# Kernel tuning notes

Hardware: AMD Instinct MI355X
Metric: run time of the kernel (lower is better)

## Reference

```python
import jax, jax.numpy as jnp
import numpy as np

B, N, HID, H, DH, NB = 4, 4096, 768, 12, 64, 266
EPS = 1e-4


def softmax_kernel(data, proj, is_query):
    # data: [B,H,N,DH], proj: [NB,DH]. FAVOR+ positive softmax features.
    d = data.shape[-1]
    ratio = proj.shape[0] ** -0.5
    dn = d ** -0.25  # data normalizer
    data_dash = jnp.einsum('bhnd,jd->bhnj', data * dn, proj)  # [B,H,N,NB]
    diag = 0.5 * jnp.sum((data * dn) ** 2, axis=-1, keepdims=True)  # [B,H,N,1]
    if is_query:
        m = jnp.max(data_dash, axis=-1, keepdims=True)
    else:
        m = jnp.max(data_dash, axis=(-1, -2), keepdims=True)
    return ratio * (jnp.exp(data_dash - diag - m) + EPS)


def setup_inputs() -> dict:
    key = jax.random.key(0)
    ks = jax.random.split(key, 8)
    s = HID ** -0.5
    return {
        'hidden_states': jax.random.normal(ks[0], (B, N, HID), jnp.float32),
        'Wq': jax.random.normal(ks[1], (HID, HID), jnp.float32) * s,
        'bq': jnp.zeros((HID,), jnp.float32),
        'Wk': jax.random.normal(ks[2], (HID, HID), jnp.float32) * s,
        'bk': jnp.zeros((HID,), jnp.float32),
        'Wv': jax.random.normal(ks[3], (HID, HID), jnp.float32) * s,
        'bv': jnp.zeros((HID,), jnp.float32),
        'proj': jax.random.normal(ks[4], (NB, DH), jnp.float32),
    }


def reference(hidden_states, Wq, bq, Wk, bk, Wv, bv, proj):
    def heads(x):  # [B,N,HID] -> [B,H,N,DH]
        return x.reshape(B, N, H, DH).transpose(0, 2, 1, 3)

    q = heads(hidden_states @ Wq.T + bq)
    k = heads(hidden_states @ Wk.T + bk)
    v = heads(hidden_states @ Wv.T + bv)

    qp = softmax_kernel(q, proj, True)   # [B,H,N,NB]
    kp = softmax_kernel(k, proj, False)  # [B,H,N,NB]

    # non-causal linear attention: out = q' (k'^T v) / (q' sum_n k')
    k_sum = jnp.sum(kp, axis=2)                               # [B,H,NB]
    d_inv = 1.0 / jnp.einsum('bhnj,bhj->bhn', qp, k_sum)      # [B,H,N]
    ctx = jnp.einsum('bhnj,bhnd->bhjd', kp, v)                # [B,H,NB,DH]
    out = jnp.einsum('bhnj,bhjd->bhnd', qp, ctx) * d_inv[..., None]

    return out.transpose(0, 2, 1, 3).reshape(B, N, HID)
```

## Files before the change

kernel.cpp:

```cpp
#include <hip/hip_runtime.h>
#include <hip/hip_bf16.h>
#include <stdint.h>

#define B_   4
#define N_   4096
#define HID_ 768
#define H_   12
#define DH_  64
#define NB_  266
#define NBP_ 288
#define EPS_ 1e-4f

typedef unsigned short u16;
typedef __attribute__((ext_vector_type(8))) short short8;
typedef __attribute__((ext_vector_type(4))) float floatx4;

__device__ __forceinline__ u16 f2b(float f) {
  __hip_bfloat16 h = __float2bfloat16(f);
  return *reinterpret_cast<u16*>(&h);
}
__device__ __forceinline__ float b2f(u16 u) {
  union { unsigned u; float f; } x; x.u = ((unsigned)u) << 16; return x.f;
}
__device__ __forceinline__ unsigned fmap(float x) {
  unsigned u = __float_as_uint(x);
  return (u & 0x80000000u) ? ~u : (u | 0x80000000u);
}
__device__ __forceinline__ float funmap(unsigned u) {
  unsigned b = (u & 0x80000000u) ? (u & 0x7FFFFFFFu) : ~u;
  return __uint_as_float(b);
}

__global__ void k_convert(const float* __restrict__ src, u16* __restrict__ dst, int n) {
  int i = blockIdx.x * blockDim.x + threadIdx.x;
  int stride = gridDim.x * blockDim.x;
  for (; i < n; i += stride) dst[i] = f2b(src[i]);
}

__global__ void k_prep_proj(const float* __restrict__ proj, u16* __restrict__ dst) {
  int i = blockIdx.x * 256 + threadIdx.x;
  if (i >= NBP_ * DH_) return;
  int j = i / DH_, d = i - j * DH_;
  float v = (j < NB_) ? proj[j * DH_ + d] * 0.35355339059327373f : 0.f;
  dst[i] = f2b(v);
}

__global__ void k_init(float* __restrict__ zf, unsigned* __restrict__ mbuf, int nf) {
  int i = blockIdx.x * 256 + threadIdx.x;
  if (i < nf) zf[i] = 0.f;
  if (i < B_ * H_) mbuf[i] = 0u;
}

__global__ __launch_bounds__(256) void k_qkv(
    const u16* __restrict__ hsb, const u16* __restrict__ wb,
    const float* __restrict__ bq, const float* __restrict__ bk, const float* __restrict__ bv,
    u16* __restrict__ qb, u16* __restrict__ kb, u16* __restrict__ vb) {
  __shared__ u16 At[128][40];
  __shared__ u16 Bt[128][40];
  const int bm = blockIdx.x, bn = blockIdx.y;
  const int m0 = bm * 128;
  const int sel = bn / 6;
  const int or0 = (bn % 6) * 128;
  const u16* W = wb + (size_t)sel * HID_ * HID_;
  const int t = threadIdx.x, lane = t & 63, wv = t >> 6;
  const int wr = (wv >> 1) * 64, wc = (wv & 1) * 64;
  const int lm = lane & 15, lq = lane >> 4;
  floatx4 acc[4][4];
#pragma unroll
  for (int i = 0; i < 4; i++)
#pragma unroll
    for (int j = 0; j < 4; j++) acc[i][j] = (floatx4){0.f, 0.f, 0.f, 0.f};

  for (int k0 = 0; k0 < HID_; k0 += 32) {
    __syncthreads();
#pragma unroll
    for (int i = 0; i < 2; i++) {
      int c = t + i * 256;
      int r = c >> 2, off = (c & 3) * 8;
      *(uint4*)&At[r][off] = *(const uint4*)(hsb + (size_t)(m0 + r) * HID_ + k0 + off);
      *(uint4*)&Bt[r][off] = *(const uint4*)(W + (size_t)(or0 + r) * HID_ + k0 + off);
    }
    __syncthreads();
    short8 af[4], bfr[4];
#pragma unroll
    for (int mt = 0; mt < 4; mt++) af[mt] = *(const short8*)&At[wr + mt * 16 + lm][lq * 8];
#pragma unroll
    for (int nt = 0; nt < 4; nt++) bfr[nt] = *(const short8*)&Bt[wc + nt * 16 + lm][lq * 8];
#pragma unroll
    for (int mt = 0; mt < 4; mt++)
#pragma unroll
      for (int nt = 0; nt < 4; nt++)
        acc[mt][nt] = __builtin_amdgcn_mfma_f32_16x16x32_bf16(af[mt], bfr[nt], acc[mt][nt], 0, 0, 0);
  }
  const float* bias = (sel == 0) ? bq : (sel == 1) ? bk : bv;
  u16* dst = (sel == 0) ? qb : (sel == 1) ? kb : vb;
#pragma unroll
  for (int mt = 0; mt < 4; mt++) {
#pragma unroll
    for (int nt = 0; nt < 4; nt++) {
      int lc = or0 + wc + nt * 16 + lm;
      float bb = bias[lc];
#pragma unroll
      for (int r = 0; r < 4; r++) {
        int row = m0 + wr + mt * 16 + lq * 4 + r;
        dst[(size_t)row * HID_ + lc] = f2b(acc[mt][nt][r] + bb);
      }
    }
  }
}

__global__ __launch_bounds__(512) void k_kmax(
    const u16* __restrict__ kb, const u16* __restrict__ projb, unsigned* __restrict__ mbuf) {
  __shared__ u16 Pl[NBP_][72];
  __shared__ u16 Kl[64][72];
  const int bh = blockIdx.y;
  const int b = bh / H_, h = bh - b * H_;
  const int n0 = blockIdx.x * 256;
  const int t = threadIdx.x, lane = t & 63, wv = t >> 6;
  const int lm = lane & 15, lq = lane >> 4;
  for (int c = t; c < NBP_ * 8; c += 512) {
    int j = c >> 3, off = (c & 7) * 8;
    *(uint4*)&Pl[j][off] = *(const uint4*)(projb + j * 64 + off);
  }
  const size_t base = ((size_t)b * N_) * HID_ + h * DH_;
  const int mt = wv >> 1, ct0 = (wv & 1) * 9;
  float mx = -3.0e38f;
  for (int s = 0; s < 4; s++) {
    __syncthreads();
    {
      int r = t >> 3, off = (t & 7) * 8;
      *(uint4*)&Kl[r][off] = *(const uint4*)(kb + base + (size_t)(n0 + s * 64 + r) * HID_ + off);
    }
    __syncthreads();
    short8 af0 = *(const short8*)&Kl[mt * 16 + lm][lq * 8];
    short8 af1 = *(const short8*)&Kl[mt * 16 + lm][32 + lq * 8];
#pragma unroll
    for (int ci = 0; ci < 9; ci++) {
      int ct = ct0 + ci;
      short8 bf0 = *(const short8*)&Pl[ct * 16 + lm][lq * 8];
      short8 bf1 = *(const short8*)&Pl[ct * 16 + lm][32 + lq * 8];
      floatx4 a = __builtin_amdgcn_mfma_f32_16x16x32_bf16(af0, bf0, (floatx4){0.f,0.f,0.f,0.f}, 0,0,0);
      a = __builtin_amdgcn_mfma_f32_16x16x32_bf16(af1, bf1, a, 0, 0, 0);
      int j = ct * 16 + lm;
      if (j < NB_) {
#pragma unroll
        for (int r = 0; r < 4; r++) mx = fmaxf(mx, a[r]);
      }
    }
  }
#pragma unroll
  for (int o = 1; o < 64; o <<= 1) mx = fmaxf(mx, __shfl_xor(mx, o));
  if (lane == 0) atomicMax(&mbuf[bh], fmap(mx));
}

__global__ __launch_bounds__(512) void k_ctx(
    const u16* __restrict__ kb, const u16* __restrict__ vbuf, const u16* __restrict__ projb,
    const unsigned* __restrict__ mbuf, float* __restrict__ ctxT, float* __restrict__ ksum) {
  __shared__ u16 Pl[NBP_][72];
  __shared__ u16 Kl[64][72];
  __shared__ u16 vT[64][72];
  __shared__ u16 kpT[NBP_][72];
  __shared__ float ksloc[NBP_];
  const int bh = blockIdx.y;
  const int b = bh / H_, h = bh - b * H_;
  const int n0 = blockIdx.x * 256;
  const int t = threadIdx.x, lane = t & 63, wv = t >> 6;
  const int lm = lane & 15, lq = lane >> 4;
  for (int c = t; c < NBP_ * 8; c += 512) {
    int j = c >> 3, off = (c & 7) * 8;
    *(uint4*)&Pl[j][off] = *(const uint4*)(projb + j * 64 + off);
  }
  for (int c = t; c < NBP_; c += 512) ksloc[c] = 0.f;
  const float m = funmap(mbuf[bh]);
  const float ratio = 0.06131393f;
  const size_t base = ((size_t)b * N_) * HID_ + h * DH_;
  const int mt = wv >> 1, ct0 = (wv & 1) * 9;
  floatx4 accc[9];
#pragma unroll
  for (int i = 0; i < 9; i++) accc[i] = (floatx4){0.f, 0.f, 0.f, 0.f};

  for (int s = 0; s < 4; s++) {
    __syncthreads();
    {
      int r = t >> 3, off = (t & 7) * 8;
      *(uint4*)&Kl[r][off] = *(const uint4*)(kb + base + (size_t)(n0 + s * 64 + r) * HID_ + off);
      uint4 vvv = *(const uint4*)(vbuf + base + (size_t)(n0 + s * 64 + r) * HID_ + off);
      const u16* pv = (const u16*)&vvv;
#pragma unroll
      for (int i = 0; i < 8; i++) vT[off + i][r] = pv[i];
    }
    __syncthreads();
    short8 af0 = *(const short8*)&Kl[mt * 16 + lm][lq * 8];
    short8 af1 = *(const short8*)&Kl[mt * 16 + lm][32 + lq * 8];
    float rs = 0.f;
#pragma unroll
    for (int i = 0; i < 8; i++) { float f = b2f(((const u16*)&af0)[i]); rs += f * f; }
#pragma unroll
    for (int i = 0; i < 8; i++) { float f = b2f(((const u16*)&af1)[i]); rs += f * f; }
    rs += __shfl_xor(rs, 16);
    rs += __shfl_xor(rs, 32);
    float dg[4];
#pragma unroll
    for (int r = 0; r < 4; r++) dg[r] = 0.0625f * __shfl(rs, lq * 4 + r);
#pragma unroll
    for (int ci = 0; ci < 9; ci++) {
      int ct = ct0 + ci;
      short8 bf0 = *(const short8*)&Pl[ct * 16 + lm][lq * 8];
      short8 bf1 = *(const short8*)&Pl[ct * 16 + lm][32 + lq * 8];
      floatx4 a = __builtin_amdgcn_mfma_f32_16x16x32_bf16(af0, bf0, (floatx4){0.f,0.f,0.f,0.f}, 0,0,0);
      a = __builtin_amdgcn_mfma_f32_16x16x32_bf16(af1, bf1, a, 0, 0, 0);
      int j = ct * 16 + lm;
      float kss = 0.f;
#pragma unroll
      for (int r = 0; r < 4; r++) {
        float val = (j < NB_) ? ratio * (__expf(a[r] - dg[r] - m) + EPS_) : 0.f;
        kss += val;
        kpT[j][mt * 16 + lq * 4 + r] = f2b(val);
      }
      kss += __shfl_xor(kss, 16);
      kss += __shfl_xor(kss, 32);
      if (lq == 0) atomicAdd(&ksloc[j], kss);
    }
    __syncthreads();
    short8 av0 = *(const short8*)&vT[mt * 16 + lm][lq * 8];
    short8 av1 = *(const short8*)&vT[mt * 16 + lm][32 + lq * 8];
#pragma unroll
    for (int ci = 0; ci < 9; ci++) {
      int ct = ct0 + ci;
      short8 bk0 = *(const short8*)&kpT[ct * 16 + lm][lq * 8];
      short8 bk1 = *(const short8*)&kpT[ct * 16 + lm][32 + lq * 8];
      accc[ci] = __builtin_amdgcn_mfma_f32_16x16x32_bf16(av0, bk0, accc[ci], 0, 0, 0);
      accc[ci] = __builtin_amdgcn_mfma_f32_16x16x32_bf16(av1, bk1, accc[ci], 0, 0, 0);
    }
  }
  __syncthreads();
  for (int c = t; c < NBP_; c += 512) atomicAdd(&ksum[(size_t)bh * NBP_ + c], ksloc[c]);
#pragma unroll
  for (int ci = 0; ci < 9; ci++) {
    int j = (ct0 + ci) * 16 + lm;
#pragma unroll
    for (int r = 0; r < 4; r++) {
      int dv = mt * 16 + lq * 4 + r;
      atomicAdd(&ctxT[((size_t)bh * 64 + dv) * NBP_ + j], accc[ci][r]);
    }
  }
}

__global__ __launch_bounds__(512) void k_out(
    const u16* __restrict__ qb, const u16* __restrict__ projb,
    const float* __restrict__ ctxT, const float* __restrict__ ksum,
    float* __restrict__ outp) {
  __shared__ u16 Pl[NBP_][72];
  __shared__ u16 Ql[64][72];
  __shared__ u16 qpl[64][296];
  __shared__ u16 cxl[64][296];
  __shared__ float ksl[NBP_];
  __shared__ unsigned rmx[64];
  __shared__ float dsum[64];
  const int bh = blockIdx.y;
  const int b = bh / H_, h = bh - b * H_;
  const int n0 = blockIdx.x * 256;
  const int t = threadIdx.x, lane = t & 63, wv = t >> 6;
  const int lm = lane & 15, lq = lane >> 4;
  for (int c = t; c < NBP_ * 8; c += 512) {
    int j = c >> 3, off = (c & 7) * 8;
    *(uint4*)&Pl[j][off] = *(const uint4*)(projb + j * 64 + off);
  }
  for (int c = t; c < 64 * NBP_; c += 512) {
    int dv = c / NBP_, j = c - dv * NBP_;
    cxl[dv][j] = f2b(ctxT[(size_t)bh * 64 * NBP_ + c]);
  }
  for (int c = t; c < NBP_; c += 512) ksl[c] = ksum[(size_t)bh * NBP_ + c];
  const float ratio = 0.06131393f;
  const size_t base = ((size_t)b * N_) * HID_ + h * DH_;
  const int mt = wv >> 1, ct0 = (wv & 1) * 9;

  for (int s = 0; s < 4; s++) {
    __syncthreads();
    {
      int r = t >> 3, off = (t & 7) * 8;
      *(uint4*)&Ql[r][off] = *(const uint4*)(qb + base + (size_t)(n0 + s * 64 + r) * HID_ + off);
    }
    if (t < 64) { rmx[t] = 0u; dsum[t] = 0.f; }
    __syncthreads();
    short8 af0 = *(const short8*)&Ql[mt * 16 + lm][lq * 8];
    short8 af1 = *(const short8*)&Ql[mt * 16 + lm][32 + lq * 8];
    float rs = 0.f;
#pragma unroll
    for (int i = 0; i < 8; i++) { float f = b2f(((const u16*)&af0)[i]); rs += f * f; }
#pragma unroll
    for (int i = 0; i < 8; i++) { float f = b2f(((const u16*)&af1)[i]); rs += f * f; }
    rs += __shfl_xor(rs, 16);
    rs += __shfl_xor(rs, 32);
    float dg[4];
#pragma unroll
    for (int r = 0; r < 4; r++) dg[r] = 0.0625f * __shfl(rs, lq * 4 + r);
    floatx4 dd[9];
    float rm[4] = {-3e38f, -3e38f, -3e38f, -3e38f};
#pragma unroll
    for (int ci = 0; ci < 9; ci++) {
      int ct = ct0 + ci;
      short8 bf0 = *(const short8*)&Pl[ct * 16 + lm][lq * 8];
      short8 bf1 = *(const short8*)&Pl[ct * 16 + lm][32 + lq * 8];
      floatx4 a = __builtin_amdgcn_mfma_f32_16x16x32_bf16(af0, bf0, (floatx4){0.f,0.f,0.f,0.f}, 0,0,0);
      a = __builtin_amdgcn_mfma_f32_16x16x32_bf16(af1, bf1, a, 0, 0, 0);
      dd[ci] = a;
      int j = ct * 16 + lm;
      if (j < NB_) {
#pragma unroll
        for (int r = 0; r < 4; r++) rm[r] = fmaxf(rm[r], a[r]);
      }
    }
#pragma unroll
    for (int o = 1; o < 16; o <<= 1) {
#pragma unroll
      for (int r = 0; r < 4; r++) rm[r] = fmaxf(rm[r], __shfl_xor(rm[r], o));
    }
    if (lm == 0) {
#pragma unroll
      for (int r = 0; r < 4; r++) atomicMax(&rmx[mt * 16 + lq * 4 + r], fmap(rm[r]));
    }
    __syncthreads();
    float dpart[4] = {0.f, 0.f, 0.f, 0.f};
    float mrow[4];
#pragma unroll
    for (int r = 0; r < 4; r++) mrow[r] = funmap(rmx[mt * 16 + lq * 4 + r]);
#pragma unroll
    for (int ci = 0; ci < 9; ci++) {
      int ct = ct0 + ci;
      int j = ct * 16 + lm;
      float ks = ksl[j];
#pragma unroll
      for (int r = 0; r < 4; r++) {
        float qpv = (j < NB_) ? ratio * (__expf(dd[ci][r] - dg[r] - mrow[r]) + EPS_) : 0.f;
        qpl[mt * 16 + lq * 4 + r][j] = f2b(qpv);
        dpart[r] += qpv * ks;
      }
    }
#pragma unroll
    for (int o = 1; o < 16; o <<= 1) {
#pragma unroll
      for (int r = 0; r < 4; r++) dpart[r] += __shfl_xor(dpart[r], o);
    }
    if (lm == 0) {
#pragma unroll
      for (int r = 0; r < 4; r++) atomicAdd(&dsum[mt * 16 + lq * 4 + r], dpart[r]);
    }
    __syncthreads();
    const int dt0 = (wv & 1) * 2;
    floatx4 ao[2];
    ao[0] = (floatx4){0.f, 0.f, 0.f, 0.f};
    ao[1] = (floatx4){0.f, 0.f, 0.f, 0.f};
#pragma unroll
    for (int ks_ = 0; ks_ < 9; ks_++) {
      short8 aq = *(const short8*)&qpl[mt * 16 + lm][ks_ * 32 + lq * 8];
#pragma unroll
      for (int dt = 0; dt < 2; dt++) {
        short8 bc = *(const short8*)&cxl[(dt0 + dt) * 16 + lm][ks_ * 32 + lq * 8];
        ao[dt] = __builtin_amdgcn_mfma_f32_16x16x32_bf16(aq, bc, ao[dt], 0, 0, 0);
      }
    }
#pragma unroll
    for (int dt = 0; dt < 2; dt++) {
#pragma unroll
      for (int r = 0; r < 4; r++) {
        int nloc = mt * 16 + lq * 4 + r;
        float di = 1.f / dsum[nloc];
        int n = n0 + s * 64 + nloc;
        int dv = (dt0 + dt) * 16 + lm;
        outp[((size_t)b * N_ + n) * HID_ + h * DH_ + dv] = ao[dt][r] * di;
      }
    }
  }
}

extern "C" void kernel_launch(void* const* d_in, const int* in_sizes, int n_in,
                              void* d_out, int out_size, void* d_ws, size_t ws_size,
                              hipStream_t stream) {
  (void)in_sizes; (void)n_in; (void)out_size; (void)ws_size;
  const float* hs   = (const float*)d_in[0];
  const float* Wq   = (const float*)d_in[1];
  const float* bq   = (const float*)d_in[2];
  const float* Wk   = (const float*)d_in[3];
  const float* bk   = (const float*)d_in[4];
  const float* Wv   = (const float*)d_in[5];
  const float* bv   = (const float*)d_in[6];
  const float* proj = (const float*)d_in[7];

  char* w = (char*)d_ws;
  u16* hsb   = (u16*)w;  w += (size_t)16384 * 768 * 2;
  u16* wb3   = (u16*)w;  w += (size_t)3 * 768 * 768 * 2;
  u16* projb = (u16*)w;  w += (size_t)NBP_ * 64 * 2;
  u16* qb    = (u16*)w;  w += (size_t)16384 * 768 * 2;
  u16* kb    = (u16*)w;  w += (size_t)16384 * 768 * 2;
  u16* vb    = (u16*)w;  w += (size_t)16384 * 768 * 2;
  float* ctxT = (float*)w; w += (size_t)48 * 64 * NBP_ * 4;
  float* ksum = (float*)w; w += (size_t)48 * NBP_ * 4;
  unsigned* mbuf = (unsigned*)w;

  hipLaunchKernelGGL(k_convert, dim3(2048), dim3(256), 0, stream, hs, hsb, 16384 * 768);
  hipLaunchKernelGGL(k_convert, dim3(576), dim3(256), 0, stream, Wq, wb3, 768 * 768);
  hipLaunchKernelGGL(k_convert, dim3(576), dim3(256), 0, stream, Wk, wb3 + 768 * 768, 768 * 768);
  hipLaunchKernelGGL(k_convert, dim3(576), dim3(256), 0, stream, Wv, wb3 + 2 * 768 * 768, 768 * 768);
  hipLaunchKernelGGL(k_prep_proj, dim3(72), dim3(256), 0, stream, proj, projb);
  int nz = 48 * 64 * NBP_ + 48 * NBP_;
  hipLaunchKernelGGL(k_init, dim3((nz + 255) / 256), dim3(256), 0, stream, ctxT, mbuf, nz);
  hipLaunchKernelGGL(k_qkv, dim3(128, 18), dim3(256), 0, stream, hsb, wb3, bq, bk, bv, qb, kb, vb);
  hipLaunchKernelGGL(k_kmax, dim3(16, 48), dim3(512), 0, stream, kb, projb, mbuf);
  hipLaunchKernelGGL(k_ctx, dim3(16, 48), dim3(512), 0, stream, kb, vb, projb, mbuf, ctxT, ksum);
  hipLaunchKernelGGL(k_out, dim3(16, 48), dim3(512), 0, stream, qb, projb, ctxT, ksum, (float*)d_out);
}
```

Baseline: 420.9 us.

## Restructure pipeline with global-to-LDS loads, transposed V/K' buffers, and split ctx kernels

Most of the pipeline is replaced. The QKV GEMM now stages tiles with global_load_lds, the float-to-bf16 conversion is vectorised, and V is pre-transposed into a separate buffer. K features are written to a global kpT buffer, and context is computed in a separate MFMA kernel that reads directly from global memory and accumulates with atomics. The output kernel keeps per-wave row max and denominator in registers rather than shared-memory atomics, and reads a bf16-converted context from global memory. This removes shared-memory syncs and staging, but adds large intermediate global traffic (kpT is about 113 MB) and extra kernel launches.

```diff
diff --git a/kernel.cpp b/kernel.cpp
--- a/kernel.cpp
+++ b/kernel.cpp
@@ -10,6 +10,7 @@
 #define NB_  266
 #define NBP_ 288
 #define EPS_ 1e-4f
+#define RATIO_ 0.06131393f
 
 typedef unsigned short u16;
 typedef __attribute__((ext_vector_type(8))) short short8;
@@ -30,11 +31,19 @@
   unsigned b = (u & 0x80000000u) ? (u & 0x7FFFFFFFu) : ~u;
   return __uint_as_float(b);
 }
-
-__global__ void k_convert(const float* __restrict__ src, u16* __restrict__ dst, int n) {
-  int i = blockIdx.x * blockDim.x + threadIdx.x;
-  int stride = gridDim.x * blockDim.x;
-  for (; i < n; i += stride) dst[i] = f2b(src[i]);
+__device__ __forceinline__ void gl16(const u16* g, u16* l) {
+  __builtin_amdgcn_global_load_lds(
+      (const __attribute__((address_space(1))) void*)g,
+      (__attribute__((address_space(3))) void*)l, 16, 0, 0);
+}
+
+__global__ void k_convert4(const float4* __restrict__ src, uint2* __restrict__ dst, int n4) {
+  int i = blockIdx.x * 256 + threadIdx.x;
+  if (i >= n4) return;
+  float4 v = src[i];
+  union { u16 s[4]; uint2 u; } pk;
+  pk.s[0] = f2b(v.x); pk.s[1] = f2b(v.y); pk.s[2] = f2b(v.z); pk.s[3] = f2b(v.w);
+  dst[i] = pk.u;
 }
 
 __global__ void k_prep_proj(const float* __restrict__ proj, u16* __restrict__ dst) {
@@ -55,16 +64,24 @@
     const u16* __restrict__ hsb, const u16* __restrict__ wb,
     const float* __restrict__ bq, const float* __restrict__ bk, const float* __restrict__ bv,
     u16* __restrict__ qb, u16* __restrict__ kb, u16* __restrict__ vb) {
-  __shared__ u16 At[128][40];
-  __shared__ u16 Bt[128][40];
-  const int bm = blockIdx.x, bn = blockIdx.y;
-  const int m0 = bm * 128;
+  __shared__ u16 At[128 * 32];
+  __shared__ u16 Bt[128 * 32];
+  const int m0 = blockIdx.x * 128;
+  const int bn = blockIdx.y;
   const int sel = bn / 6;
   const int or0 = (bn % 6) * 128;
   const u16* W = wb + (size_t)sel * HID_ * HID_;
   const int t = threadIdx.x, lane = t & 63, wv = t >> 6;
   const int wr = (wv >> 1) * 64, wc = (wv & 1) * 64;
   const int lm = lane & 15, lq = lane >> 4;
+  const int srow = wv * 32 + (lane >> 2);
+  const int scol = (lane & 3) * 8;
+  const u16* gA0 = hsb + (size_t)(m0 + srow) * HID_ + scol;
+  const u16* gA1 = gA0 + 16 * HID_;
+  const u16* gB0 = W + (size_t)(or0 + srow) * HID_ + scol;
+  const u16* gB1 = gB0 + 16 * HID_;
+  u16* lA = At + wv * 1024;
+  u16* lB = Bt + wv * 1024;
   floatx4 acc[4][4];
 #pragma unroll
   for (int i = 0; i < 4; i++)
@@ -73,19 +90,16 @@
 
   for (int k0 = 0; k0 < HID_; k0 += 32) {
     __syncthreads();
-#pragma unroll
-    for (int i = 0; i < 2; i++) {
-      int c = t + i * 256;
-      int r = c >> 2, off = (c & 3) * 8;
-      *(uint4*)&At[r][off] = *(const uint4*)(hsb + (size_t)(m0 + r) * HID_ + k0 + off);
-      *(uint4*)&Bt[r][off] = *(const uint4*)(W + (size_t)(or0 + r) * HID_ + k0 + off);
-    }
+    gl16(gA0 + k0, lA);
+    gl16(gA1 + k0, lA + 512);
+    gl16(gB0 + k0, lB);
+    gl16(gB1 + k0, lB + 512);
     __syncthreads();
     short8 af[4], bfr[4];
 #pragma unroll
-    for (int mt = 0; mt < 4; mt++) af[mt] = *(const short8*)&At[wr + mt * 16 + lm][lq * 8];
-#pragma unroll
-    for (int nt = 0; nt < 4; nt++) bfr[nt] = *(const short8*)&Bt[wc + nt * 16 + lm][lq * 8];
+    for (int mt = 0; mt < 4; mt++) af[mt] = *(const short8*)&At[(wr + mt * 16 + lm) * 32 + lq * 8];
+#pragma unroll
+    for (int nt = 0; nt < 4; nt++) bfr[nt] = *(const short8*)&Bt[(wc + nt * 16 + lm) * 32 + lq * 8];
 #pragma unroll
     for (int mt = 0; mt < 4; mt++)
 #pragma unroll
@@ -109,40 +123,58 @@
   }
 }
 
-__global__ __launch_bounds__(512) void k_kmax(
+__global__ __launch_bounds__(256) void k_vt(const u16* __restrict__ vb, u16* __restrict__ vT) {
+  __shared__ u16 tile[64][72];
+  const int bh = blockIdx.y, b = bh / H_, h = bh - b * H_;
+  const int nc = blockIdx.x * 64;
+  const int t = threadIdx.x;
+#pragma unroll
+  for (int i = 0; i < 2; i++) {
+    int lin = t + i * 256;
+    int r = lin >> 3, c8 = (lin & 7) * 8;
+    *(uint4*)&tile[r][c8] = *(const uint4*)(vb + (size_t)(b * N_ + nc + r) * HID_ + h * DH_ + c8);
+  }
+  __syncthreads();
+#pragma unroll
+  for (int i = 0; i < 2; i++) {
+    int lin = t + i * 256;
+    int dv = lin >> 3, c8 = (lin & 7) * 8;
+    union { u16 s[8]; uint4 u; } pk;
+#pragma unroll
+    for (int k = 0; k < 8; k++) {
+      int p = c8 + k, blk = p >> 5, q = p & 31;
+      int nl = blk * 32 + ((q >> 2) & 1) * 16 + (q >> 3) * 4 + (q & 3);
+      pk.s[k] = tile[nl][dv];
+    }
+    *(uint4*)(vT + ((size_t)bh * DH_ + dv) * N_ + nc + c8) = pk.u;
+  }
+}
+
+__global__ __launch_bounds__(256) void k_kmax2(
     const u16* __restrict__ kb, const u16* __restrict__ projb, unsigned* __restrict__ mbuf) {
-  __shared__ u16 Pl[NBP_][72];
-  __shared__ u16 Kl[64][72];
-  const int bh = blockIdx.y;
-  const int b = bh / H_, h = bh - b * H_;
+  const int bh = blockIdx.y, b = bh / H_, h = bh - b * H_;
   const int n0 = blockIdx.x * 256;
   const int t = threadIdx.x, lane = t & 63, wv = t >> 6;
   const int lm = lane & 15, lq = lane >> 4;
-  for (int c = t; c < NBP_ * 8; c += 512) {
-    int j = c >> 3, off = (c & 7) * 8;
-    *(uint4*)&Pl[j][off] = *(const uint4*)(projb + j * 64 + off);
-  }
-  const size_t base = ((size_t)b * N_) * HID_ + h * DH_;
-  const int mt = wv >> 1, ct0 = (wv & 1) * 9;
-  float mx = -3.0e38f;
-  for (int s = 0; s < 4; s++) {
-    __syncthreads();
-    {
-      int r = t >> 3, off = (t & 7) * 8;
-      *(uint4*)&Kl[r][off] = *(const uint4*)(kb + base + (size_t)(n0 + s * 64 + r) * HID_ + off);
-    }
-    __syncthreads();
-    short8 af0 = *(const short8*)&Kl[mt * 16 + lm][lq * 8];
-    short8 af1 = *(const short8*)&Kl[mt * 16 + lm][32 + lq * 8];
-#pragma unroll
-    for (int ci = 0; ci < 9; ci++) {
-      int ct = ct0 + ci;
-      short8 bf0 = *(const short8*)&Pl[ct * 16 + lm][lq * 8];
-      short8 bf1 = *(const short8*)&Pl[ct * 16 + lm][32 + lq * 8];
-      floatx4 a = __builtin_amdgcn_mfma_f32_16x16x32_bf16(af0, bf0, (floatx4){0.f,0.f,0.f,0.f}, 0,0,0);
-      a = __builtin_amdgcn_mfma_f32_16x16x32_bf16(af1, bf1, a, 0, 0, 0);
-      int j = ct * 16 + lm;
-      if (j < NB_) {
+  const u16* kbase = kb + (size_t)(b * N_ + n0 + wv * 64) * HID_ + h * DH_;
+  short8 af0[4], af1[4];
+#pragma unroll
+  for (int mt = 0; mt < 4; mt++) {
+    const u16* p = kbase + (size_t)(mt * 16 + lm) * HID_ + lq * 8;
+    af0[mt] = *(const short8*)p;
+    af1[mt] = *(const short8*)(p + 32);
+  }
+  float mx = -3e38f;
+  for (int ct = 0; ct < 17; ct++) {
+    const u16* pp = projb + (ct * 16 + lm) * DH_ + lq * 8;
+    short8 bf0 = *(const short8*)pp;
+    short8 bf1 = *(const short8*)(pp + 32);
+    bool valid = (ct < 16) || (lm < 10);
+#pragma unroll
+    for (int mt = 0; mt < 4; mt++) {
+      floatx4 a = __builtin_amdgcn_mfma_f32_16x16x32_bf16(af0[mt], bf0, (floatx4){0.f,0.f,0.f,0.f}, 0, 0, 0);
+      a = __builtin_amdgcn_mfma_f32_16x16x32_bf16(af1[mt], bf1, a, 0, 0, 0);
+      if (valid) {
 #pragma unroll
         for (int r = 0; r < 4; r++) mx = fmaxf(mx, a[r]);
       }
@@ -153,45 +185,128 @@
   if (lane == 0) atomicMax(&mbuf[bh], fmap(mx));
 }
 
-__global__ __launch_bounds__(512) void k_ctx(
-    const u16* __restrict__ kb, const u16* __restrict__ vbuf, const u16* __restrict__ projb,
-    const unsigned* __restrict__ mbuf, float* __restrict__ ctxT, float* __restrict__ ksum) {
-  __shared__ u16 Pl[NBP_][72];
-  __shared__ u16 Kl[64][72];
-  __shared__ u16 vT[64][72];
-  __shared__ u16 kpT[NBP_][72];
-  __shared__ float ksloc[NBP_];
-  const int bh = blockIdx.y;
-  const int b = bh / H_, h = bh - b * H_;
+__global__ __launch_bounds__(256) void k_kp(
+    const u16* __restrict__ kb, const u16* __restrict__ projb, const unsigned* __restrict__ mbuf,
+    u16* __restrict__ kpT, float* __restrict__ ksum) {
+  const int bh = blockIdx.y, b = bh / H_, h = bh - b * H_;
   const int n0 = blockIdx.x * 256;
   const int t = threadIdx.x, lane = t & 63, wv = t >> 6;
   const int lm = lane & 15, lq = lane >> 4;
-  for (int c = t; c < NBP_ * 8; c += 512) {
-    int j = c >> 3, off = (c & 7) * 8;
-    *(uint4*)&Pl[j][off] = *(const uint4*)(projb + j * 64 + off);
-  }
-  for (int c = t; c < NBP_; c += 512) ksloc[c] = 0.f;
   const float m = funmap(mbuf[bh]);
-  const float ratio = 0.06131393f;
-  const size_t base = ((size_t)b * N_) * HID_ + h * DH_;
-  const int mt = wv >> 1, ct0 = (wv & 1) * 9;
-  floatx4 accc[9];
-#pragma unroll
-  for (int i = 0; i < 9; i++) accc[i] = (floatx4){0.f, 0.f, 0.f, 0.f};
-
-  for (int s = 0; s < 4; s++) {
-    __syncthreads();
-    {
-      int r = t >> 3, off = (t & 7) * 8;
-      *(uint4*)&Kl[r][off] = *(const uint4*)(kb + base + (size_t)(n0 + s * 64 + r) * HID_ + off);
-      uint4 vvv = *(const uint4*)(vbuf + base + (size_t)(n0 + s * 64 + r) * HID_ + off);
-      const u16* pv = (const u16*)&vvv;
-#pragma unroll
-      for (int i = 0; i < 8; i++) vT[off + i][r] = pv[i];
-    }
-    __syncthreads();
-    short8 af0 = *(const short8*)&Kl[mt * 16 + lm][lq * 8];
-    short8 af1 = *(const short8*)&Kl[mt * 16 + lm][32 + lq * 8];
+  const u16* kbase = kb + (size_t)(b * N_ + n0 + wv * 64) * HID_ + h * DH_;
+  const size_t kpbase = (size_t)bh * NBP_ * N_;
+  const int nw = n0 + wv * 64;
+  float kacc[18];
+#pragma unroll
+  for (int ct = 0; ct < 18; ct++) kacc[ct] = 0.f;
+  uint2 stash[18];
+
+  for (int pair = 0; pair < 2; pair++) {
+#pragma unroll
+    for (int sub = 0; sub < 2; sub++) {
+      const int mt = pair * 2 + sub;
+      const u16* prow = kbase + (size_t)(mt * 16 + lm) * HID_ + lq * 8;
+      short8 af0 = *(const short8*)prow;
+      short8 af1 = *(const short8*)(prow + 32);
+      float rs = 0.f;
+#pragma unroll
+      for (int i = 0; i < 8; i++) { float f = b2f(((const u16*)&af0)[i]); rs += f * f; }
+#pragma unroll
+      for (int i = 0; i < 8; i++) { float f = b2f(((const u16*)&af1)[i]); rs += f * f; }
+      rs += __shfl_xor(rs, 16);
+      rs += __shfl_xor(rs, 32);
+      float dg[4];
+#pragma unroll
+      for (int r = 0; r < 4; r++) dg[r] = 0.0625f * __shfl(rs, lq * 4 + r);
+#pragma unroll
+      for (int ct = 0; ct < 18; ct++) {
+        floatx4 a;
+        if (ct < 17) {
+          const u16* pp = projb + (ct * 16 + lm) * DH_ + lq * 8;
+          short8 bf0 = *(const short8*)pp;
+          short8 bf1 = *(const short8*)(pp + 32);
+          a = __builtin_amdgcn_mfma_f32_16x16x32_bf16(af0, bf0, (floatx4){0.f,0.f,0.f,0.f}, 0, 0, 0);
+          a = __builtin_amdgcn_mfma_f32_16x16x32_bf16(af1, bf1, a, 0, 0, 0);
+        } else {
+          a = (floatx4){0.f, 0.f, 0.f, 0.f};
+        }
+        bool valid = (ct < 16) || (ct == 16 && lm < 10);
+        union { u16 s[4]; uint2 u; } pk;
+        float kss = 0.f;
+#pragma unroll
+        for (int r = 0; r < 4; r++) {
+          float val = valid ? RATIO_ * (__expf(a[r] - dg[r] - m) + EPS_) : 0.f;
+          kss += val;
+          pk.s[r] = f2b(val);
+        }
+        kacc[ct] += kss;
+        if (sub == 0) {
+          stash[ct] = pk.u;
+        } else {
+          uint4 w4 = make_uint4(stash[ct].x, stash[ct].y, pk.u.x, pk.u.y);
+          *(uint4*)(kpT + kpbase + (size_t)(ct * 16 + lm) * N_ + nw + pair * 32 + lq * 8) = w4;
+        }
+      }
+    }
+  }
+#pragma unroll
+  for (int ct = 0; ct < 18; ct++) {
+    float v = kacc[ct];
+    v += __shfl_xor(v, 16);
+    v += __shfl_xor(v, 32);
+    if (lq == 0) atomicAdd(&ksum[bh * NBP_ + ct * 16 + lm], v);
+  }
+}
+
+__global__ __launch_bounds__(256) void k_ctx2(
+    const u16* __restrict__ vT, const u16* __restrict__ kpT, float* __restrict__ ctxTf) {
+  const int bh = blockIdx.y;
+  const int kc = blockIdx.x * 256;
+  const int t = threadIdx.x, lane = t & 63, wv = t >> 6;
+  const int lm = lane & 15, lq = lane >> 4;
+  const u16* Ab = vT + ((size_t)bh * DH_ + wv * 16 + lm) * N_ + kc + lq * 8;
+  const u16* Bb = kpT + (size_t)bh * NBP_ * N_ + kc + lq * 8;
+  floatx4 acc[18];
+#pragma unroll
+  for (int ct = 0; ct < 18; ct++) acc[ct] = (floatx4){0.f, 0.f, 0.f, 0.f};
+  for (int ks = 0; ks < 8; ks++) {
+    short8 av = *(const short8*)(Ab + ks * 32);
+#pragma unroll
+    for (int ct = 0; ct < 18; ct++) {
+      short8 bv = *(const short8*)(Bb + (size_t)(ct * 16 + lm) * N_ + ks * 32);
+      acc[ct] = __builtin_amdgcn_mfma_f32_16x16x32_bf16(av, bv, acc[ct], 0, 0, 0);
+    }
+  }
+#pragma unroll
+  for (int ct = 0; ct < 18; ct++) {
+#pragma unroll
+    for (int r = 0; r < 4; r++)
+      atomicAdd(&ctxTf[((size_t)bh * DH_ + wv * 16 + lq * 4 + r) * NBP_ + ct * 16 + lm], acc[ct][r]);
+  }
+}
+
+__global__ void k_cvt_ctx(const float* __restrict__ src, u16* __restrict__ dst) {
+  int i = blockIdx.x * 256 + threadIdx.x;
+  if (i < B_ * H_ * DH_ * NBP_) dst[i] = f2b(src[i]);
+}
+
+__global__ __launch_bounds__(256) void k_out2(
+    const u16* __restrict__ qb, const u16* __restrict__ projb,
+    const u16* __restrict__ ctxb, const float* __restrict__ ksum,
+    float* __restrict__ outp) {
+  __shared__ u16 qpl[4][16][296];
+  const int bh = blockIdx.y, b = bh / H_, h = bh - b * H_;
+  const int n0 = blockIdx.x * 256;
+  const int t = threadIdx.x, lane = t & 63, wv = t >> 6;
+  const int lm = lane & 15, lq = lane >> 4;
+  const u16* qbase = qb + (size_t)(b * N_ + n0 + wv * 64) * HID_ + h * DH_;
+  const u16* cb = ctxb + (size_t)bh * DH_ * NBP_;
+  const float* ksb = ksum + bh * NBP_;
+
+  for (int mt = 0; mt < 4; mt++) {
+    const u16* prow = qbase + (size_t)(mt * 16 + lm) * HID_ + lq * 8;
+    short8 af0 = *(const short8*)prow;
+    short8 af1 = *(const short8*)(prow + 32);
     float rs = 0.f;
 #pragma unroll
     for (int i = 0; i < 8; i++) { float f = b2f(((const u16*)&af0)[i]); rs += f * f; }
@@ -202,173 +317,67 @@
     float dg[4];
 #pragma unroll
     for (int r = 0; r < 4; r++) dg[r] = 0.0625f * __shfl(rs, lq * 4 + r);
-#pragma unroll
-    for (int ci = 0; ci < 9; ci++) {
-      int ct = ct0 + ci;
-      short8 bf0 = *(const short8*)&Pl[ct * 16 + lm][lq * 8];
-      short8 bf1 = *(const short8*)&Pl[ct * 16 + lm][32 + lq * 8];
-      floatx4 a = __builtin_amdgcn_mfma_f32_16x16x32_bf16(af0, bf0, (floatx4){0.f,0.f,0.f,0.f}, 0,0,0);
+
+    floatx4 dd[17];
+    float rm[4] = {-3e38f, -3e38f, -3e38f, -3e38f};
+#pragma unroll
+    for (int ct = 0; ct < 17; ct++) {
+      const u16* pp = projb + (ct * 16 + lm) * DH_ + lq * 8;
+      short8 bf0 = *(const short8*)pp;
+      short8 bf1 = *(const short8*)(pp + 32);
+      floatx4 a = __builtin_amdgcn_mfma_f32_16x16x32_bf16(af0, bf0, (floatx4){0.f,0.f,0.f,0.f}, 0, 0, 0);
       a = __builtin_amdgcn_mfma_f32_16x16x32_bf16(af1, bf1, a, 0, 0, 0);
-      int j = ct * 16 + lm;
-      float kss = 0.f;
+      dd[ct] = a;
+      if ((ct < 16) || (lm < 10)) {
+#pragma unroll
+        for (int r = 0; r < 4; r++) rm[r] = fmaxf(rm[r], a[r]);
+      }
+    }
+#pragma unroll
+    for (int o = 1; o < 16; o <<= 1) {
+#pragma unroll
+      for (int r = 0; r < 4; r++) rm[r] = fmaxf(rm[r], __shfl_xor(rm[r], o));
+    }
+    float dpart[4] = {0.f, 0.f, 0.f, 0.f};
+#pragma unroll
+    for (int ct = 0; ct < 18; ct++) {
+      floatx4 a = (ct < 17) ? dd[ct] : (floatx4){0.f, 0.f, 0.f, 0.f};
+      bool valid = (ct < 16) || (ct == 16 && lm < 10);
+      float ksv = ksb[ct * 16 + lm];
 #pragma unroll
       for (int r = 0; r < 4; r++) {
-        float val = (j < NB_) ? ratio * (__expf(a[r] - dg[r] - m) + EPS_) : 0.f;
-        kss += val;
-        kpT[j][mt * 16 + lq * 4 + r] = f2b(val);
-      }
-      kss += __shfl_xor(kss, 16);
-      kss += __shfl_xor(kss, 32);
-      if (lq == 0) atomicAdd(&ksloc[j], kss);
-    }
-    __syncthreads();
-    short8 av0 = *(const short8*)&vT[mt * 16 + lm][lq * 8];
-    short8 av1 = *(const short8*)&vT[mt * 16 + lm][32 + lq * 8];
-#pragma unroll
-    for (int ci = 0; ci < 9; ci++) {
-      int ct = ct0 + ci;
-      short8 bk0 = *(const short8*)&kpT[ct * 16 + lm][lq * 8];
-      short8 bk1 = *(const short8*)&kpT[ct * 16 + lm][32 + lq * 8];
-      accc[ci] = __builtin_amdgcn_mfma_f32_16x16x32_bf16(av0, bk0, accc[ci], 0, 0, 0);
-      accc[ci] = __builtin_amdgcn_mfma_f32_16x16x32_bf16(av1, bk1, accc[ci], 0, 0, 0);
-    }
-  }
-  __syncthreads();
-  for (int c = t; c < NBP_; c += 512) atomicAdd(&ksum[(size_t)bh * NBP_ + c], ksloc[c]);
-#pragma unroll
-  for (int ci = 0; ci < 9; ci++) {
-    int j = (ct0 + ci) * 16 + lm;
-#pragma unroll
-    for (int r = 0; r < 4; r++) {
-      int dv = mt * 16 + lq * 4 + r;
-      atomicAdd(&ctxT[((size_t)bh * 64 + dv) * NBP_ + j], accc[ci][r]);
-    }
-  }
-}
-
-__global__ __launch_bounds__(512) void k_out(
-    const u16* __restrict__ qb, const u16* __restrict__ projb,
-    const float* __restrict__ ctxT, const float* __restrict__ ksum,
-    float* __restrict__ outp) {
-  __shared__ u16 Pl[NBP_][72];
-  __shared__ u16 Ql[64][72];
-  __shared__ u16 qpl[64][296];
-  __shared__ u16 cxl[64][296];
-  __shared__ float ksl[NBP_];
-  __shared__ unsigned rmx[64];
-  __shared__ float dsum[64];
-  const int bh = blockIdx.y;
-  const int b = bh / H_, h = bh - b * H_;
-  const int n0 = blockIdx.x * 256;
-  const int t = threadIdx.x, lane = t & 63, wv = t >> 6;
-  const int lm = lane & 15, lq = lane >> 4;
-  for (int c = t; c < NBP_ * 8; c += 512) {
-    int j = c >> 3, off = (c & 7) * 8;
-    *(uint4*)&Pl[j][off] = *(const uint4*)(projb + j * 64 + off);
-  }
-  for (int c = t; c < 64 * NBP_; c += 512) {
-    int dv = c / NBP_, j = c - dv * NBP_;
-    cxl[dv][j] = f2b(ctxT[(size_t)bh * 64 * NBP_ + c]);
-  }
-  for (int c = t; c < NBP_; c += 512) ksl[c] = ksum[(size_t)bh * NBP_ + c];
-  const float ratio = 0.06131393f;
-  const size_t base = ((size_t)b * N_) * HID_ + h * DH_;
-  const int mt = wv >> 1, ct0 = (wv & 1) * 9;
-
-  for (int s = 0; s < 4; s++) {
-    __syncthreads();
-    {
-      int r = t >> 3, off = (t & 7) * 8;
-      *(uint4*)&Ql[r][off] = *(const uint4*)(qb + base + (size_t)(n0 + s * 64 + r) * HID_ + off);
-    }
-    if (t < 64) { rmx[t] = 0u; dsum[t] = 0.f; }
-    __syncthreads();
-    short8 af0 = *(const short8*)&Ql[mt * 16 + lm][lq * 8];
-    short8 af1 = *(const short8*)&Ql[mt * 16 + lm][32 + lq * 8];
-    float rs = 0.f;
-#pragma unroll
-    for (int i = 0; i < 8; i++) { float f = b2f(((const u16*)&af0)[i]); rs += f * f; }
-#pragma unroll
-    for (int i = 0; i < 8; i++) { float f = b2f(((const u16*)&af1)[i]); rs += f * f; }
-    rs += __shfl_xor(rs, 16);
-    rs += __shfl_xor(rs, 32);
-    float dg[4];
-#pragma unroll
-    for (int r = 0; r < 4; r++) dg[r] = 0.0625f * __shfl(rs, lq * 4 + r);
-    floatx4 dd[9];
-    float rm[4] = {-3e38f, -3e38f, -3e38f, -3e38f};
-#pragma unroll
-    for (int ci = 0; ci < 9; ci++) {
-      int ct = ct0 + ci;
-      short8 bf0 = *(const short8*)&Pl[ct * 16 + lm][lq * 8];
-      short8 bf1 = *(const short8*)&Pl[ct * 16 + lm][32 + lq * 8];
-      floatx4 a = __builtin_amdgcn_mfma_f32_16x16x32_bf16(af0, bf0, (floatx4){0.f,0.f,0.f,0.f}, 0,0,0);
-      a = __builtin_amdgcn_mfma_f32_16x16x32_bf16(af1, bf1, a, 0, 0, 0);
-      dd[ci] = a;
-      int j = ct * 16 + lm;
-      if (j < NB_) {
-#pragma unroll
-        for (int r = 0; r < 4; r++) rm[r] = fmaxf(rm[r], a[r]);
+        float qpv = valid ? RATIO_ * (__expf(a[r] - dg[r] - rm[r]) + EPS_) : 0.f;
+        dpart[r] += qpv * ksv;
+        qpl[wv][lq * 4 + r][ct * 16 + lm] = f2b(qpv);
       }
     }
 #pragma unroll
     for (int o = 1; o < 16; o <<= 1) {
 #pragma unroll
-      for (int r = 0; r < 4; r++) rm[r] = fmaxf(rm[r], __shfl_xor(rm[r], o));
-    }
-    if (lm == 0) {
-#pragma unroll
-      for (int r = 0; r < 4; r++) atomicMax(&rmx[mt * 16 + lq * 4 + r], fmap(rm[r]));
-    }
-    __syncthreads();
-    float dpart[4] = {0.f, 0.f, 0.f, 0.f};
-    float mrow[4];
-#pragma unroll
-    for (int r = 0; r < 4; r++) mrow[r] = funmap(rmx[mt * 16 + lq * 4 + r]);
-#pragma unroll
-    for (int ci = 0; ci < 9; ci++) {
-      int ct = ct0 + ci;
-      int j = ct * 16 + lm;
-      float ks = ksl[j];
+      for (int r = 0; r < 4; r++) dpart[r] += __shfl_xor(dpart[r], o);
+    }
+    float dinv[4];
+#pragma unroll
+    for (int r = 0; r < 4; r++) dinv[r] = 1.f / dpart[r];
+
+    floatx4 ao[4];
+#pragma unroll
+    for (int dt = 0; dt < 4; dt++) ao[dt] = (floatx4){0.f, 0.f, 0.f, 0.f};
+#pragma unroll
+    for (int ks9 = 0; ks9 < 9; ks9++) {
+      short8 aq = *(const short8*)&qpl[wv][lm][ks9 * 32 + lq * 8];
+#pragma unroll
+      for (int dt = 0; dt < 4; dt++) {
+        short8 bc = *(const short8*)(cb + (size_t)(dt * 16 + lm) * NBP_ + ks9 * 32 + lq * 8);
+        ao[dt] = __builtin_amdgcn_mfma_f32_16x16x32_bf16(aq, bc, ao[dt], 0, 0, 0);
+      }
+    }
+#pragma unroll
+    for (int dt = 0; dt < 4; dt++) {
 #pragma unroll
       for (int r = 0; r < 4; r++) {
-        float qpv = (j < NB_) ? ratio * (__expf(dd[ci][r] - dg[r] - mrow[r]) + EPS_) : 0.f;
-        qpl[mt * 16 + lq * 4 + r][j] = f2b(qpv);
-        dpart[r] += qpv * ks;
-      }
-    }
-#pragma unroll
-    for (int o = 1; o < 16; o <<= 1) {
-#pragma unroll
-      for (int r = 0; r < 4; r++) dpart[r] += __shfl_xor(dpart[r], o);
-    }
-    if (lm == 0) {
-#pragma unroll
-      for (int r = 0; r < 4; r++) atomicAdd(&dsum[mt * 16 + lq * 4 + r], dpart[r]);
-    }
-    __syncthreads();
-    const int dt0 = (wv & 1) * 2;
-    floatx4 ao[2];
-    ao[0] = (floatx4){0.f, 0.f, 0.f, 0.f};
-    ao[1] = (floatx4){0.f, 0.f, 0.f, 0.f};
-#pragma unroll
-    for (int ks_ = 0; ks_ < 9; ks_++) {
-      short8 aq = *(const short8*)&qpl[mt * 16 + lm][ks_ * 32 + lq * 8];
-#pragma unroll
-      for (int dt = 0; dt < 2; dt++) {
-        short8 bc = *(const short8*)&cxl[(dt0 + dt) * 16 + lm][ks_ * 32 + lq * 8];
-        ao[dt] = __builtin_amdgcn_mfma_f32_16x16x32_bf16(aq, bc, ao[dt], 0, 0, 0);
-      }
-    }
-#pragma unroll
-    for (int dt = 0; dt < 2; dt++) {
-#pragma unroll
-      for (int r = 0; r < 4; r++) {
-        int nloc = mt * 16 + lq * 4 + r;
-        float di = 1.f / dsum[nloc];
-        int n = n0 + s * 64 + nloc;
-        int dv = (dt0 + dt) * 16 + lm;
-        outp[((size_t)b * N_ + n) * HID_ + h * DH_ + dv] = ao[dt][r] * di;
+        int n = n0 + wv * 64 + mt * 16 + lq * 4 + r;
+        outp[((size_t)(b * N_ + n)) * HID_ + h * DH_ + dt * 16 + lm] = ao[dt][r] * dinv[r];
       }
     }
   }
@@ -394,19 +403,25 @@
   u16* qb    = (u16*)w;  w += (size_t)16384 * 768 * 2;
   u16* kb    = (u16*)w;  w += (size_t)16384 * 768 * 2;
   u16* vb    = (u16*)w;  w += (size_t)16384 * 768 * 2;
-  float* ctxT = (float*)w; w += (size_t)48 * 64 * NBP_ * 4;
-  float* ksum = (float*)w; w += (size_t)48 * NBP_ * 4;
+  u16* kpT   = (u16*)w;  w += (size_t)48 * NBP_ * N_ * 2;
+  float* ksum  = (float*)w; w += (size_t)48 * NBP_ * 4;
+  float* ctxTf = (float*)w; w += (size_t)48 * DH_ * NBP_ * 4;
+  u16* ctxTb = (u16*)w;  w += (size_t)48 * DH_ * NBP_ * 2;
   unsigned* mbuf = (unsigned*)w;
-
-  hipLaunchKernelGGL(k_convert, dim3(2048), dim3(256), 0, stream, hs, hsb, 16384 * 768);
-  hipLaunchKernelGGL(k_convert, dim3(576), dim3(256), 0, stream, Wq, wb3, 768 * 768);
-  hipLaunchKernelGGL(k_convert, dim3(576), dim3(256), 0, stream, Wk, wb3 + 768 * 768, 768 * 768);
-  hipLaunchKernelGGL(k_convert, dim3(576), dim3(256), 0, stream, Wv, wb3 + 2 * 768 * 768, 768 * 768);
+  u16* vT = hsb;
+
+  hipLaunchKernelGGL(k_convert4, dim3(12288), dim3(256), 0, stream, (const float4*)hs, (uint2*)hsb, 16384 * 768 / 4);
+  hipLaunchKernelGGL(k_convert4, dim3(576), dim3(256), 0, stream, (const float4*)Wq, (uint2*)wb3, 768 * 768 / 4);
+  hipLaunchKernelGGL(k_convert4, dim3(576), dim3(256), 0, stream, (const float4*)Wk, (uint2*)(wb3 + 768 * 768), 768 * 768 / 4);
+  hipLaunchKernelGGL(k_convert4, dim3(576), dim3(256), 0, stream, (const float4*)Wv, (uint2*)(wb3 + 2 * 768 * 768), 768 * 768 / 4);
   hipLaunchKernelGGL(k_prep_proj, dim3(72), dim3(256), 0, stream, proj, projb);
-  int nz = 48 * 64 * NBP_ + 48 * NBP_;
-  hipLaunchKernelGGL(k_init, dim3((nz + 255) / 256), dim3(256), 0, stream, ctxT, mbuf, nz);
+  int nz = 48 * NBP_ + 48 * DH_ * NBP_;
+  hipLaunchKernelGGL(k_init, dim3((nz + 255) / 256), dim3(256), 0, stream, ksum, mbuf, nz);
   hipLaunchKernelGGL(k_qkv, dim3(128, 18), dim3(256), 0, stream, hsb, wb3, bq, bk, bv, qb, kb, vb);
-  hipLaunchKernelGGL(k_kmax, dim3(16, 48), dim3(512), 0, stream, kb, projb, mbuf);
-  hipLaunchKernelGGL(k_ctx, dim3(16, 48), dim3(512), 0, stream, kb, vb, projb, mbuf, ctxT, ksum);
-  hipLaunchKernelGGL(k_out, dim3(16, 48), dim3(512), 0, stream, qb, projb, ctxT, ksum, (float*)d_out);
-}
+  hipLaunchKernelGGL(k_vt, dim3(64, 48), dim3(256), 0, stream, vb, vT);
+  hipLaunchKernelGGL(k_kmax2, dim3(16, 48), dim3(256), 0, stream, kb, projb, mbuf);
+  hipLaunchKernelGGL(k_kp, dim3(16, 48), dim3(256), 0, stream, kb, projb, mbuf, kpT, ksum);
+  hipLaunchKernelGGL(k_ctx2, dim3(16, 48), dim3(256), 0, stream, vT, kpT, ctxTf);
+  hipLaunchKernelGGL(k_cvt_ctx, dim3((48 * DH_ * NBP_ + 255) / 256), dim3(256), 0, stream, ctxTf, ctxTb);
+  hipLaunchKernelGGL(k_out2, dim3(16, 48), dim3(256), 0, stream, qb, projb, ctxTb, ksum, (float*)d_out);
+}
```

New measurement: 457.0 us. +8.6%, slower.
